# Kernel tuning notes

Hardware: AMD Instinct MI355X
Metric: run time of the kernel (lower is better)

Reference implementation:

```python
import jax, jax.numpy as jnp
import numpy as np


def _fake_quant(x, num_bits):
    # Per-tensor uniform min/max fake quantization with STE (straight-through).
    qmax = float(2 ** num_bits - 1)
    mn = jnp.min(x)
    mx = jnp.max(x)
    scale = (mx - mn) / qmax
    q = jnp.round((x - mn) / scale) * scale + mn
    return x + jax.lax.stop_gradient(q - x)


def _qlinear(x, W, b, num_bits):
    xq = _fake_quant(x, num_bits)
    Wq = _fake_quant(W, num_bits)
    return xq @ Wq.T + b


def setup_inputs() -> dict:
    key = jax.random.key(0)
    ks = jax.random.split(key, 7)
    B, D, H = 8192, 1024, 1024
    s = 1.0 / np.sqrt(H)
    return {
        "input": jax.random.normal(ks[0], (B, D), jnp.float32),
        "h": jax.random.normal(ks[1], (B, H), jnp.float32),
        "c": jax.random.normal(ks[2], (B, H), jnp.float32),
        "W_in": jax.random.normal(ks[3], (4 * H, D), jnp.float32) * s,
        "b_in": jax.random.normal(ks[4], (4 * H,), jnp.float32) * s,
        "W_h": jax.random.normal(ks[5], (4 * H, H), jnp.float32) * s,
        "b_h": jax.random.normal(ks[6], (4 * H,), jnp.float32) * s,
        "num_bits": 8,
        "num_bits_grad": 8,
    }


def reference(input, h, c, W_in, b_in, W_h, b_h, num_bits, num_bits_grad):
    B = input.shape[0]
    Hd = h.shape[1]
    mixed_input = _qlinear(input, W_in, b_in, num_bits).reshape(B, 4, Hd)
    mixed_hidden = _qlinear(h, W_h, b_h, num_bits).reshape(B, 4, Hd)
    gates = mixed_input + mixed_hidden  # [B, 4, H]
    i = jax.nn.sigmoid(gates[:, 0, :])
    f = jax.nn.sigmoid(gates[:, 1, :])
    g = jnp.tanh(gates[:, 2, :])
    o = jax.nn.sigmoid(gates[:, 3, :])
    c_ = f * c + i * g
    h_ = o * jnp.tanh(c_)
    return (h_, c_)
```

## Files before the change

### kernel.cpp

```cpp
#include <hip/hip_runtime.h>
#include <hip/hip_bf16.h>

typedef unsigned short u16;
typedef int i32x4 __attribute__((ext_vector_type(4)));
typedef int i32x16 __attribute__((ext_vector_type(16)));
typedef signed char s8;

#define NB_RED 256

static __device__ __forceinline__ float tanh_fast(float x) {
    float t = __expf(2.0f * x);
    return 1.0f - 2.0f / (t + 1.0f);
}

__global__ void k_minmax_partial(const float* __restrict__ x, const float* __restrict__ h,
                                 const float* __restrict__ wi, const float* __restrict__ wh,
                                 float* __restrict__ partials) {
    int t = blockIdx.y;
    const float* p = (t == 0) ? x : (t == 1) ? h : (t == 2) ? wi : wh;
    int n4 = ((t < 2) ? (8192 * 1024) : (4096 * 1024)) >> 2;
    float mn = 3.4e38f, mx = -3.4e38f;
    const float4* p4 = (const float4*)p;
    for (int i = blockIdx.x * blockDim.x + threadIdx.x; i < n4; i += gridDim.x * blockDim.x) {
        float4 v = p4[i];
        mn = fminf(mn, fminf(fminf(v.x, v.y), fminf(v.z, v.w)));
        mx = fmaxf(mx, fmaxf(fmaxf(v.x, v.y), fmaxf(v.z, v.w)));
    }
    for (int d = 1; d < 64; d <<= 1) {
        mn = fminf(mn, __shfl_xor(mn, d));
        mx = fmaxf(mx, __shfl_xor(mx, d));
    }
    __shared__ float smn[4], smx[4];
    int wv = threadIdx.x >> 6;
    if ((threadIdx.x & 63) == 0) { smn[wv] = mn; smx[wv] = mx; }
    __syncthreads();
    if (threadIdx.x == 0) {
        mn = fminf(fminf(smn[0], smn[1]), fminf(smn[2], smn[3]));
        mx = fmaxf(fmaxf(smx[0], smx[1]), fmaxf(smx[2], smx[3]));
        partials[(t * NB_RED + blockIdx.x) * 2 + 0] = mn;
        partials[(t * NB_RED + blockIdx.x) * 2 + 1] = mx;
    }
}

__global__ void k_minmax_final(const float* __restrict__ partials, const int* __restrict__ nbits,
                               float* __restrict__ params) {
    int t = blockIdx.x;
    int tid = threadIdx.x;
    float mn = partials[(t * NB_RED + tid) * 2 + 0];
    float mx = partials[(t * NB_RED + tid) * 2 + 1];
    for (int d = 1; d < 64; d <<= 1) {
        mn = fminf(mn, __shfl_xor(mn, d));
        mx = fmaxf(mx, __shfl_xor(mx, d));
    }
    __shared__ float smn[4], smx[4];
    int wv = tid >> 6;
    if ((tid & 63) == 0) { smn[wv] = mn; smx[wv] = mx; }
    __syncthreads();
    if (tid == 0) {
        mn = fminf(fminf(smn[0], smn[1]), fminf(smn[2], smn[3]));
        mx = fmaxf(fmaxf(smx[0], smx[1]), fmaxf(smx[2], smx[3]));
        float qmax = (float)((1u << (*nbits)) - 1u);
        params[t * 2 + 0] = mn;
        params[t * 2 + 1] = (mx - mn) / qmax;
    }
}

static __device__ __forceinline__ int block_reduce_i(int v, int tid) {
    for (int d = 1; d < 64; d <<= 1) v += __shfl_xor(v, d);
    __shared__ int sred[4];
    if ((tid & 63) == 0) sred[tid >> 6] = v;
    __syncthreads();
    return sred[0] + sred[1] + sred[2] + sred[3];
}

__global__ void k_quant(const float* __restrict__ x, const float* __restrict__ h,
                        const float* __restrict__ wi, const float* __restrict__ wh,
                        const float* __restrict__ params,
                        const float* __restrict__ b_in, const float* __restrict__ b_h,
                        s8* __restrict__ A8, s8* __restrict__ W8,
                        float* __restrict__ Rax, float* __restrict__ Rah,
                        float* __restrict__ Rbi, float* __restrict__ Rbh,
                        float* __restrict__ bc) {
    int b = blockIdx.x;
    int t = threadIdx.x;
    if (b < 16384) {
        int tsel = b >> 13;
        int row = b & 8191;
        const float* src = tsel ? h : x;
        float mn = params[tsel * 2 + 0], s = params[tsel * 2 + 1];
        float4 v = ((const float4*)(src + (size_t)row * 1024))[t];
        int k0 = (int)fminf(255.f, fmaxf(0.f, rintf((v.x - mn) / s)));
        int k1 = (int)fminf(255.f, fmaxf(0.f, rintf((v.y - mn) / s)));
        int k2 = (int)fminf(255.f, fmaxf(0.f, rintf((v.z - mn) / s)));
        int k3 = (int)fminf(255.f, fmaxf(0.f, rintf((v.w - mn) / s)));
        unsigned p = ((unsigned)((k0 - 128) & 0xff)) | ((unsigned)((k1 - 128) & 0xff) << 8) |
                     ((unsigned)((k2 - 128) & 0xff) << 16) | ((unsigned)((k3 - 128) & 0xff) << 24);
        *(unsigned*)(A8 + (size_t)row * 2048 + tsel * 1024 + t * 4) = p;
        int sum = block_reduce_i(k0 + k1 + k2 + k3 - 512, t);
        if (t == 0) (tsel ? Rah : Rax)[row] = (float)sum;
    } else if (b < 24576) {
        int bb = b - 16384;
        int tsel = bb >> 12;
        int row = bb & 4095;
        const float* src = tsel ? wh : wi;
        float mn = params[(2 + tsel) * 2 + 0], s = params[(2 + tsel) * 2 + 1];
        int g = row >> 10, j = row & 1023;
        int prow = (j >> 5) * 128 + g * 32 + (j & 31);
        float4 v = ((const float4*)(src + (size_t)row * 1024))[t];
        int k0 = (int)fminf(255.f, fmaxf(0.f, rintf((v.x - mn) / s)));
        int k1 = (int)fminf(255.f, fmaxf(0.f, rintf((v.y - mn) / s)));
        int k2 = (int)fminf(255.f, fmaxf(0.f, rintf((v.z - mn) / s)));
        int k3 = (int)fminf(255.f, fmaxf(0.f, rintf((v.w - mn) / s)));
        unsigned p = ((unsigned)((k0 - 128) & 0xff)) | ((unsigned)((k1 - 128) & 0xff) << 8) |
                     ((unsigned)((k2 - 128) & 0xff) << 16) | ((unsigned)((k3 - 128) & 0xff) << 24);
        *(unsigned*)(W8 + (size_t)prow * 2048 + tsel * 1024 + t * 4) = p;
        int sum = block_reduce_i(k0 + k1 + k2 + k3 - 512, t);
        if (t == 0) (tsel ? Rbh : Rbi)[prow] = (float)sum;
    } else {
        int n = (b - 24576) * 256 + t;
        int j = (n >> 7) * 32 + (n & 31);
        int g = (n >> 5) & 3;
        bc[n] = b_in[g * 1024 + j] + b_h[g * 1024 + j];
    }
}

__global__ __launch_bounds__(512, 4) void k_gemm_lstm(
    const s8* __restrict__ A8, const s8* __restrict__ W8,
    const float* __restrict__ params, const float* __restrict__ bc,
    const float* __restrict__ Rax, const float* __restrict__ Rah,
    const float* __restrict__ Rbi, const float* __restrict__ Rbh,
    const float* __restrict__ c_in, float* __restrict__ out) {
    __shared__ __align__(16) s8 As[3][8192];
    __shared__ __align__(16) s8 Bs[3][16384];

    const int tid = threadIdx.x;
    const int wave = tid >> 6, lane = tid & 63;
    const int wr = wave >> 1, wc = wave & 1;
    const int l31 = lane & 31, lh = lane >> 5;

    const int bid = blockIdx.x;
    const int l = bid >> 3;
    const int bx = l >> 3;
    const int by = (bid & 7) * 8 + (l & 7);
    const int bm = by * 128, bn = bx * 256;

    const int skb = (((tid & 3) ^ ((tid >> 3) & 3) ^ ((tid >> 5) & 3)) * 16);
    const int q = ((l31 >> 1) ^ (l31 >> 3)) & 3;

    const float sa = params[1], sh = params[3], si = params[5], sw = params[7];
    const float csx = sa * si, csh = sh * sw;
    const float r = csx / csh;

    const s8* pA0 = A8 + (size_t)(bm + (tid >> 2)) * 2048 + skb;
    const s8* pB0 = W8 + (size_t)(bn + (tid >> 2)) * 2048 + skb;
    const s8* pB1 = pB0 + (size_t)128 * 2048;

    i32x16 acc[4];
#pragma unroll
    for (int f = 0; f < 4; f++) acc[f] = (i32x16)0;

#define STAGE(B, T)                                                                               \
    do {                                                                                          \
        __builtin_amdgcn_global_load_lds(                                                         \
            (const __attribute__((address_space(1))) void*)(pA0 + (T) * 64),                      \
            (__attribute__((address_space(3))) void*)&As[(B)][tid * 16], 16, 0, 0);               \
        __builtin_amdgcn_global_load_lds(                                                         \
            (const __attribute__((address_space(1))) void*)(pB0 + (T) * 64),                      \
            (__attribute__((address_space(3))) void*)&Bs[(B)][tid * 16], 16, 0, 0);               \
        __builtin_amdgcn_global_load_lds(                                                         \
            (const __attribute__((address_space(1))) void*)(pB1 + (T) * 64),                      \
            (__attribute__((address_space(3))) void*)&Bs[(B)][8192 + tid * 16], 16, 0, 0);        \
    } while (0)

#define COMPUTE(B)                                                                                \
    do {                                                                                          \
        _Pragma("unroll") for (int ks = 0; ks < 2; ++ks) {                                        \
            const int ro = ((ks * 2 + lh) ^ q) * 16;                                              \
            i32x4 a = *(const i32x4*)&As[(B)][(wr * 32 + l31) * 64 + ro];                         \
            i32x4 bf;                                                                             \
            _Pragma("unroll") for (int f = 0; f < 4; ++f) {                                       \
                bf = *(const i32x4*)&Bs[(B)][(wc * 128 + f * 32 + l31) * 64 + ro];                \
                acc[f] = __builtin_amdgcn_mfma_i32_32x32x32_i8(a, bf, acc[f], 0, 0, 0);           \
            }                                                                                     \
        }                                                                                         \
    } while (0)

    STAGE(0, 0);
    STAGE(1, 1);
    asm volatile("s_waitcnt vmcnt(3)" ::: "memory");
    __builtin_amdgcn_s_barrier();

#pragma unroll
    for (int t = 0; t < 32; ++t) {
        if (t < 30) STAGE((t + 2) % 3, t + 2);
        if (t == 16) {
#pragma unroll
            for (int f = 0; f < 4; f++)
#pragma unroll
                for (int e = 0; e < 16; e++)
                    acc[f][e] = (int)rintf((float)acc[f][e] * r);
        }
        COMPUTE(t % 3);
        if (t < 30) { asm volatile("s_waitcnt vmcnt(3)" ::: "memory"); }
        else if (t == 30) { asm volatile("s_waitcnt vmcnt(0)" ::: "memory"); }
        if (t < 31) __builtin_amdgcn_s_barrier();
    }

#undef STAGE
#undef COMPUTE

    float mna = params[0], mnh = params[2], mni = params[4], mnw = params[6];
    float za = mna + 128.0f * sa, zi = mni + 128.0f * si;
    float zh = mnh + 128.0f * sh, zw = mnw + 128.0f * sw;
    float C0 = 1024.0f * (za * zi + zh * zw);
    float cax = sa * zi, cah = sh * zw;
    float cbx = si * za, cbh = sw * zh;

    const int nb = bn + wc * 128;
    float colt[4];
#pragma unroll
    for (int f = 0; f < 4; ++f) {
        int np = nb + f * 32 + l31;
        colt[f] = bc[np] + cbx * Rbi[np] + cbh * Rbh[np] + C0;
    }
    const int ub = (nb >> 7) * 32 + l31;

#pragma unroll
    for (int reg = 0; reg < 16; reg++) {
        int row = bm + wr * 32 + (reg & 3) + 8 * (reg >> 2) + 4 * lh;
        float rterm = cax * Rax[row] + cah * Rah[row];
        float g0 = colt[0] + rterm + csh * (float)acc[0][reg];
        float g1 = colt[1] + rterm + csh * (float)acc[1][reg];
        float g2 = colt[2] + rterm + csh * (float)acc[2][reg];
        float g3 = colt[3] + rterm + csh * (float)acc[3][reg];
        float iv = 1.0f / (1.0f + __expf(-g0));
        float fv = 1.0f / (1.0f + __expf(-g1));
        float gv = tanh_fast(g2);
        float ov = 1.0f / (1.0f + __expf(-g3));
        size_t off = (size_t)row * 1024 + ub;
        float cv = c_in[off];
        float cn = fv * cv + iv * gv;
        float hn = ov * tanh_fast(cn);
        out[off] = hn;
        out[(size_t)8192 * 1024 + off] = cn;
    }
}

extern "C" void kernel_launch(void* const* d_in, const int* in_sizes, int n_in,
                              void* d_out, int out_size, void* d_ws, size_t ws_size,
                              hipStream_t stream) {
    const float* x = (const float*)d_in[0];
    const float* h = (const float*)d_in[1];
    const float* c = (const float*)d_in[2];
    const float* wi = (const float*)d_in[3];
    const float* bi = (const float*)d_in[4];
    const float* wh = (const float*)d_in[5];
    const float* bh = (const float*)d_in[6];
    const int* nbits = (const int*)d_in[7];
    float* out = (float*)d_out;

    char* ws = (char*)d_ws;
    float* params   = (float*)ws;
    float* partials = (float*)(ws + 64);
    float* bc  = (float*)(ws + 16384);
    float* Rax = (float*)(ws + 32768);
    float* Rah = (float*)(ws + 65536);
    float* Rbi = (float*)(ws + 98304);
    float* Rbh = (float*)(ws + 114688);
    s8* A8 = (s8*)(ws + 131072);
    s8* W8 = (s8*)(ws + 131072 + (size_t)16 * 1024 * 1024);

    k_minmax_partial<<<dim3(NB_RED, 4), 256, 0, stream>>>(x, h, wi, wh, partials);
    k_minmax_final<<<4, 256, 0, stream>>>(partials, nbits, params);
    k_quant<<<24592, 256, 0, stream>>>(x, h, wi, wh, params, bi, bh,
                                       A8, W8, Rax, Rah, Rbi, Rbh, bc);
    k_gemm_lstm<<<1024, 512, 0, stream>>>(A8, W8, params, bc, Rax, Rah, Rbi, Rbh, c, out);
}
```

Baseline: 136.3 us.

## Use 2x2 MFMA warp tiles with LDS exchange of gate accumulators in epilogue

Changes the per-wave tiling from 32x128 (one A fragment, four B fragments) to 64x64 (two A and two B fragments), so fewer LDS fragment reads are needed per MFMA. Because one wave no longer holds all four gates for a column, the weight row permutation and bias layout are changed, and neighbouring waves swap half of their accumulators through shared memory before the LSTM epilogue. This adds two barriers and an LDS round trip in the epilogue. The register footprint stays about the same.

New measurement: 135.3 us, median of 2. Within noise of the previous version (-0.7%).

```diff
diff --git a/kernel.cpp b/kernel.cpp
--- a/kernel.cpp
+++ b/kernel.cpp
@@ -105,7 +105,7 @@
         const float* src = tsel ? wh : wi;
         float mn = params[(2 + tsel) * 2 + 0], s = params[(2 + tsel) * 2 + 1];
         int g = row >> 10, j = row & 1023;
-        int prow = (j >> 5) * 128 + g * 32 + (j & 31);
+        int prow = (j >> 6) * 256 + ((j >> 5) & 1) * 128 + g * 32 + (j & 31);
         float4 v = ((const float4*)(src + (size_t)row * 1024))[t];
         int k0 = (int)fminf(255.f, fmaxf(0.f, rintf((v.x - mn) / s)));
         int k1 = (int)fminf(255.f, fmaxf(0.f, rintf((v.y - mn) / s)));
@@ -118,8 +118,9 @@
         if (t == 0) (tsel ? Rbh : Rbi)[prow] = (float)sum;
     } else {
         int n = (b - 24576) * 256 + t;
-        int j = (n >> 7) * 32 + (n & 31);
-        int g = (n >> 5) & 3;
+        int tIdx = n >> 8, c = n & 255;
+        int j = tIdx * 64 + ((c >> 7) & 1) * 32 + (c & 31);
+        int g = (c >> 5) & 3;
         bc[n] = b_in[g * 1024 + j] + b_h[g * 1024 + j];
     }
 }
@@ -130,12 +131,13 @@
     const float* __restrict__ Rax, const float* __restrict__ Rah,
     const float* __restrict__ Rbi, const float* __restrict__ Rbh,
     const float* __restrict__ c_in, float* __restrict__ out) {
-    __shared__ __align__(16) s8 As[3][8192];
-    __shared__ __align__(16) s8 Bs[3][16384];
+    __shared__ __align__(16) s8 SH[73728];
+#define ASB(B) (SH + (B) * 8192)
+#define BSB(B) (SH + 24576 + (B) * 16384)
 
     const int tid = threadIdx.x;
     const int wave = tid >> 6, lane = tid & 63;
-    const int wr = wave >> 1, wc = wave & 1;
+    const int wr = wave >> 2, wc = wave & 3;
     const int l31 = lane & 31, lh = lane >> 5;
 
     const int bid = blockIdx.x;
@@ -155,33 +157,37 @@
     const s8* pB0 = W8 + (size_t)(bn + (tid >> 2)) * 2048 + skb;
     const s8* pB1 = pB0 + (size_t)128 * 2048;
 
-    i32x16 acc[4];
-#pragma unroll
-    for (int f = 0; f < 4; f++) acc[f] = (i32x16)0;
+    i32x16 acc[2][2];
+#pragma unroll
+    for (int m = 0; m < 2; m++)
+#pragma unroll
+        for (int n = 0; n < 2; n++) acc[m][n] = (i32x16)0;
 
 #define STAGE(B, T)                                                                               \
     do {                                                                                          \
         __builtin_amdgcn_global_load_lds(                                                         \
             (const __attribute__((address_space(1))) void*)(pA0 + (T) * 64),                      \
-            (__attribute__((address_space(3))) void*)&As[(B)][tid * 16], 16, 0, 0);               \
+            (__attribute__((address_space(3))) void*)(ASB(B) + tid * 16), 16, 0, 0);              \
         __builtin_amdgcn_global_load_lds(                                                         \
             (const __attribute__((address_space(1))) void*)(pB0 + (T) * 64),                      \
-            (__attribute__((address_space(3))) void*)&Bs[(B)][tid * 16], 16, 0, 0);               \
+            (__attribute__((address_space(3))) void*)(BSB(B) + tid * 16), 16, 0, 0);              \
         __builtin_amdgcn_global_load_lds(                                                         \
             (const __attribute__((address_space(1))) void*)(pB1 + (T) * 64),                      \
-            (__attribute__((address_space(3))) void*)&Bs[(B)][8192 + tid * 16], 16, 0, 0);        \
+            (__attribute__((address_space(3))) void*)(BSB(B) + 8192 + tid * 16), 16, 0, 0);       \
     } while (0)
 
 #define COMPUTE(B)                                                                                \
     do {                                                                                          \
         _Pragma("unroll") for (int ks = 0; ks < 2; ++ks) {                                        \
             const int ro = ((ks * 2 + lh) ^ q) * 16;                                              \
-            i32x4 a = *(const i32x4*)&As[(B)][(wr * 32 + l31) * 64 + ro];                         \
-            i32x4 bf;                                                                             \
-            _Pragma("unroll") for (int f = 0; f < 4; ++f) {                                       \
-                bf = *(const i32x4*)&Bs[(B)][(wc * 128 + f * 32 + l31) * 64 + ro];                \
-                acc[f] = __builtin_amdgcn_mfma_i32_32x32x32_i8(a, bf, acc[f], 0, 0, 0);           \
-            }                                                                                     \
+            i32x4 a0 = *(const i32x4*)(ASB(B) + (wr * 64 + l31) * 64 + ro);                       \
+            i32x4 a1 = *(const i32x4*)(ASB(B) + (wr * 64 + 32 + l31) * 64 + ro);                  \
+            i32x4 b0 = *(const i32x4*)(BSB(B) + (wc * 64 + l31) * 64 + ro);                       \
+            i32x4 b1 = *(const i32x4*)(BSB(B) + (wc * 64 + 32 + l31) * 64 + ro);                  \
+            acc[0][0] = __builtin_amdgcn_mfma_i32_32x32x32_i8(a0, b0, acc[0][0], 0, 0, 0);        \
+            acc[0][1] = __builtin_amdgcn_mfma_i32_32x32x32_i8(a0, b1, acc[0][1], 0, 0, 0);        \
+            acc[1][0] = __builtin_amdgcn_mfma_i32_32x32x32_i8(a1, b0, acc[1][0], 0, 0, 0);        \
+            acc[1][1] = __builtin_amdgcn_mfma_i32_32x32x32_i8(a1, b1, acc[1][1], 0, 0, 0);        \
         }                                                                                         \
     } while (0)
 
@@ -195,10 +201,12 @@
         if (t < 30) STAGE((t + 2) % 3, t + 2);
         if (t == 16) {
 #pragma unroll
-            for (int f = 0; f < 4; f++)
-#pragma unroll
-                for (int e = 0; e < 16; e++)
-                    acc[f][e] = (int)rintf((float)acc[f][e] * r);
+            for (int m = 0; m < 2; m++)
+#pragma unroll
+                for (int n = 0; n < 2; n++)
+#pragma unroll
+                    for (int e = 0; e < 16; e++)
+                        acc[m][n][e] = (int)rintf((float)acc[m][n][e] * r);
         }
         COMPUTE(t % 3);
         if (t < 30) { asm volatile("s_waitcnt vmcnt(3)" ::: "memory"); }
@@ -208,6 +216,30 @@
 
 #undef STAGE
 #undef COMPUTE
+
+    __syncthreads();
+
+    const int P = wc & 1;
+    const int l7 = lane & 7;
+    s8* xw = SH + wave * 8192 + lane * 128;
+    s8* xr = SH + (wave ^ 1) * 8192 + lane * 128;
+
+#define WRX(MIP)                                                              \
+    do {                                                                      \
+        _Pragma("unroll") for (int ni = 0; ni < 2; ++ni)                      \
+            _Pragma("unroll") for (int c2 = 0; c2 < 4; ++c2) {                \
+                i32x4 v;                                                      \
+                v[0] = acc[MIP][ni][4 * c2 + 0];                              \
+                v[1] = acc[MIP][ni][4 * c2 + 1];                              \
+                v[2] = acc[MIP][ni][4 * c2 + 2];                              \
+                v[3] = acc[MIP][ni][4 * c2 + 3];                              \
+                *(i32x4*)(xw + (((ni * 4 + c2) ^ l7) * 16)) = v;              \
+            }                                                                 \
+    } while (0)
+    if (P == 0) WRX(1); else WRX(0);
+#undef WRX
+
+    __syncthreads();
 
     float mna = params[0], mnh = params[2], mni = params[4], mnw = params[6];
     float za = mna + 128.0f * sa, zi = mni + 128.0f * si;
@@ -216,34 +248,53 @@
     float cax = sa * zi, cah = sh * zw;
     float cbx = si * za, cbh = sw * zh;
 
-    const int nb = bn + wc * 128;
     float colt[4];
 #pragma unroll
-    for (int f = 0; f < 4; ++f) {
-        int np = nb + f * 32 + l31;
-        colt[f] = bc[np] + cbx * Rbi[np] + cbh * Rbh[np] + C0;
-    }
-    const int ub = (nb >> 7) * 32 + l31;
-
-#pragma unroll
-    for (int reg = 0; reg < 16; reg++) {
-        int row = bm + wr * 32 + (reg & 3) + 8 * (reg >> 2) + 4 * lh;
-        float rterm = cax * Rax[row] + cah * Rah[row];
-        float g0 = colt[0] + rterm + csh * (float)acc[0][reg];
-        float g1 = colt[1] + rterm + csh * (float)acc[1][reg];
-        float g2 = colt[2] + rterm + csh * (float)acc[2][reg];
-        float g3 = colt[3] + rterm + csh * (float)acc[3][reg];
-        float iv = 1.0f / (1.0f + __expf(-g0));
-        float fv = 1.0f / (1.0f + __expf(-g1));
-        float gv = tanh_fast(g2);
-        float ov = 1.0f / (1.0f + __expf(-g3));
-        size_t off = (size_t)row * 1024 + ub;
-        float cv = c_in[off];
-        float cn = fv * cv + iv * gv;
-        float hn = ov * tanh_fast(cn);
-        out[off] = hn;
-        out[(size_t)8192 * 1024 + off] = cn;
-    }
+    for (int g = 0; g < 4; ++g) {
+        int np = bn + (wc >> 1) * 128 + g * 32 + l31;
+        colt[g] = bc[np] + cbx * Rbi[np] + cbh * Rbh[np] + C0;
+    }
+    const int ub = (bn >> 2) + (wc >> 1) * 32 + l31;
+
+#define EPI(MIO)                                                              \
+    do {                                                                      \
+        _Pragma("unroll") for (int c2 = 0; c2 < 4; ++c2) {                    \
+            i32x4 q0 = *(const i32x4*)(xr + (((c2) ^ l7) * 16));              \
+            i32x4 q1 = *(const i32x4*)(xr + (((4 + c2) ^ l7) * 16));          \
+            _Pragma("unroll") for (int e = 0; e < 4; ++e) {                   \
+                int row = bm + wr * 64 + (MIO) * 32 + 8 * c2 + 4 * lh + e;    \
+                float rterm = cax * Rax[row] + cah * Rah[row];                \
+                float gv0, gv1, gv2, gv3;                                     \
+                if ((MIO) == 0) {                                             \
+                    gv0 = (float)acc[0][0][4 * c2 + e];                       \
+                    gv1 = (float)acc[0][1][4 * c2 + e];                       \
+                    gv2 = (float)q0[e]; gv3 = (float)q1[e];                   \
+                } else {                                                      \
+                    gv2 = (float)acc[1][0][4 * c2 + e];                       \
+                    gv3 = (float)acc[1][1][4 * c2 + e];                       \
+                    gv0 = (float)q0[e]; gv1 = (float)q1[e];                   \
+                }                                                             \
+                float g0 = colt[0] + rterm + csh * gv0;                       \
+                float g1 = colt[1] + rterm + csh * gv1;                       \
+                float g2 = colt[2] + rterm + csh * gv2;                       \
+                float g3 = colt[3] + rterm + csh * gv3;                       \
+                float iv = 1.0f / (1.0f + __expf(-g0));                       \
+                float fv = 1.0f / (1.0f + __expf(-g1));                       \
+                float gg = tanh_fast(g2);                                     \
+                float ov = 1.0f / (1.0f + __expf(-g3));                       \
+                size_t off = (size_t)row * 1024 + ub;                         \
+                float cv = c_in[off];                                         \
+                float cn = fv * cv + iv * gg;                                 \
+                float hn = ov * tanh_fast(cn);                                \
+                out[off] = hn;                                                \
+                out[(size_t)8192 * 1024 + off] = cn;                          \
+            }                                                                 \
+        }                                                                     \
+    } while (0)
+    if (P == 0) EPI(0); else EPI(1);
+#undef EPI
+#undef ASB
+#undef BSB
 }
 
 extern "C" void kernel_launch(void* const* d_in, const int* in_sizes, int n_in,
```
